# Performance work log

Measured on AMD Instinct MI355X. Metric: run time of the kernel, lower is better.

Reference implementation:

```python
import jax, jax.numpy as jnp
import numpy as np

B, C_IN, H, W = 2, 32, 512, 512
HIDDEN, SIZE = 768, 16
LATENT, NUM_CLASS = 128, 21
HP, WP = H // SIZE, W // SIZE
EPS = 1e-8
TEMP = 0.5


def setup_inputs() -> dict:
    key = jax.random.key(0)
    k1, k2, k3, k4, k5 = jax.random.split(key, 5)
    x = jax.random.normal(k1, (B, C_IN, H, W), dtype=jnp.float32)
    mask = jax.random.randint(k2, (B, NUM_CLASS, HP, WP), 0, 2).astype(jnp.int32)
    conv_w = jax.random.normal(k3, (HIDDEN, C_IN, SIZE, SIZE), dtype=jnp.float32) * 0.02
    conv_b = jax.random.normal(k4, (HIDDEN,), dtype=jnp.float32) * 0.02
    latent = jax.random.normal(k5, (1, LATENT * NUM_CLASS, HIDDEN), dtype=jnp.float32)
    return {"x": x, "mask": mask, "conv_w": conv_w, "conv_b": conv_b, "latent": latent}


def reference(x, mask, conv_w, conv_b, latent):
    # Patch embedding: Conv2d(kernel=stride=16) -> (B, HIDDEN, HP, WP)
    patch = jax.lax.conv_general_dilated(
        x, conv_w, window_strides=(SIZE, SIZE), padding='VALID',
        dimension_numbers=('NCHW', 'OIHW', 'NCHW'))
    patch = patch + conv_b[None, :, None, None]
    Bv = x.shape[0]
    N = HP * WP
    patch = patch.reshape(Bv, HIDDEN, N).transpose(0, 2, 1)  # (B, N, D)
    lat = jnp.broadcast_to(latent, (Bv, LATENT * NUM_CLASS, HIDDEN))  # (B, LC, D)

    # Cosine similarity as normalized batched matmul (same math as
    # torch CosineSimilarity over broadcast (B, LC, N, D))
    dots = jnp.einsum('bld,bnd->bln', lat, patch)  # (B, LC, N)
    lat_norm = jnp.linalg.norm(lat, axis=-1)       # (B, LC)
    pat_norm = jnp.linalg.norm(patch, axis=-1)     # (B, N)
    sim = dots / jnp.maximum(lat_norm[:, :, None] * pat_norm[:, None, :], EPS)

    sim = sim.reshape(Bv, LATENT, NUM_CLASS, HP, WP).mean(axis=1)  # (B, C, HP, WP)

    m = mask.astype(jnp.float32) >= 0.5
    s = jnp.sum(jnp.where(m, jnp.exp(sim / TEMP), 0.0))
    return -jnp.log(s)
```

## Files before the change

kernel.cpp:

```cpp
#include <hip/hip_runtime.h>
#include <math.h>

#define B_     2
#define CIN    32
#define HH     512
#define WW     512
#define HID    768
#define SZ     16
#define NPATCH 1024
#define KDIM   8192
#define NCLS   21
#define LAT    128
#define LC     2688
#define NP     (B_ * NPATCH)

#define NB_W4  1536
#define NB_XT  2048

typedef __attribute__((ext_vector_type(8))) short short8;
typedef __attribute__((ext_vector_type(4))) float f32x4;

__device__ __forceinline__ ushort f2bf(float f) {
    union { float f; unsigned u; } v; v.f = f;
    unsigned r = (v.u + 0x7fff + ((v.u >> 16) & 1)) >> 16;
    return (ushort)r;
}
__device__ __forceinline__ float bf2f(ushort u) {
    union { unsigned u; float f; } v; v.u = (unsigned)u << 16;
    return v.f;
}

__device__ __forceinline__ void gload16(const void* g, void* l) {
    __builtin_amdgcn_global_load_lds(
        (const __attribute__((address_space(1))) unsigned int*)g,
        (__attribute__((address_space(3))) unsigned int*)l, 16, 0, 0);
}

__global__ __launch_bounds__(256) void k_prep(const float* __restrict__ w,
                                              const float* __restrict__ x,
                                              const float* __restrict__ lat,
                                              ushort* __restrict__ wb,
                                              ushort* __restrict__ xb,
                                              float* __restrict__ classlat) {
    const int bid = blockIdx.x;
    const int t   = threadIdx.x;

    if (bid < NB_W4) {
#pragma unroll
        for (int k = 0; k < 4; ++k) {
            size_t i = ((size_t)bid * 1024 + k * 256 + t) * 4;
            float4 v = *(const float4*)(w + i);
            ushort4 o;
            o.x = f2bf(v.x); o.y = f2bf(v.y); o.z = f2bf(v.z); o.w = f2bf(v.w);
            *(ushort4*)(wb + i) = o;
        }
    } else if (bid < NB_W4 + NB_XT) {
        __shared__ ushort sh[32 * 264];
        const int cvb = bid - NB_W4;
        const int b  = cvb >> 10;
        const int c  = (cvb >> 5) & 31;
        const int ph = cvb & 31;
        const float* src = x + (((size_t)(b * CIN + c) * HH) + (size_t)ph * 16) * WW;

#pragma unroll
        for (int q = 0; q < 8; ++q) {
            int f  = q * 256 + t;
            int i  = f >> 7;
            int w4 = f & 127;
            float4 v = *(const float4*)(src + (size_t)i * WW + w4 * 4);
            int pw = w4 >> 2, j0 = (w4 & 3) * 4;
            ushort4 o;
            o.x = f2bf(v.x); o.y = f2bf(v.y); o.z = f2bf(v.z); o.w = f2bf(v.w);
            *(ushort4*)&sh[pw * 264 + i * 16 + j0] = o;
        }
        __syncthreads();

        ushort* dst = xb + ((size_t)(b * 1024 + ph * 32) << 13) + c * 256;
#pragma unroll
        for (int q = 0; q < 4; ++q) {
            int s  = q * 256 + t;
            int pw = s >> 5;
            int o8 = (s & 31) * 8;
            short8 v = *(const short8*)&sh[pw * 264 + o8];
            *(short8*)&dst[((size_t)pw << 13) + o8] = v;
        }
    } else {
        const int cls  = bid - (NB_W4 + NB_XT);
        const int lane = t & 63, wv = t >> 6;
        __shared__ float sc_sh[LAT];

        for (int q = 0; q < 32; q += 2) {
            int u0 = wv * 32 + q;
            const float* r0 = lat + (size_t)(u0 * NCLS + cls) * HID;
            const float* r1 = lat + (size_t)((u0 + 1) * NCLS + cls) * HID;
            float s0 = 0.f, s1 = 0.f;
#pragma unroll
            for (int e = 0; e < HID / 64; ++e) {
                float a = r0[lane + e * 64]; s0 += a * a;
                float b2 = r1[lane + e * 64]; s1 += b2 * b2;
            }
#pragma unroll
            for (int off = 32; off >= 1; off >>= 1) {
                s0 += __shfl_xor(s0, off, 64);
                s1 += __shfl_xor(s1, off, 64);
            }
            if (lane == 0) {
                sc_sh[u0]     = 1.0f / (128.0f * sqrtf(s0));
                sc_sh[u0 + 1] = 1.0f / (128.0f * sqrtf(s1));
            }
        }
        __syncthreads();

        float a0 = 0.f, a1 = 0.f, a2 = 0.f;
#pragma unroll 4
        for (int u = 0; u < LAT; ++u) {
            float sc = sc_sh[u];
            const float* row = lat + (size_t)(u * NCLS + cls) * HID;
            a0 += row[t] * sc;
            a1 += row[t + 256] * sc;
            a2 += row[t + 512] * sc;
        }
        classlat[cls * HID + t]       = a0;
        classlat[cls * HID + t + 256] = a1;
        classlat[cls * HID + t + 512] = a2;
    }
}

template <int SPLITK>
__global__ __launch_bounds__(256) void k_gemm(const ushort* __restrict__ xb,
                                              const ushort* __restrict__ wb,
                                              ushort* __restrict__ pbuf) {
    constexpr int KS = KDIM / SPLITK;
    __shared__ ushort Als[128 * 64];
    __shared__ ushort Bls[128 * 64];

    const int flat = blockIdx.x + 16 * (blockIdx.y + 6 * blockIdx.z);
    constexpr int nwg = 96 * SPLITK;
    const int wg = (flat & 7) * (nwg >> 3) + (flat >> 3);
    const int bz = wg / 96;
    const int rr = wg - bz * 96;
    const int by = rr % 6;
    const int bx = rr / 6;

    const int tid  = threadIdx.x;
    const int wv   = tid >> 6;
    const int lane = tid & 63;
    const int wm   = (wv >> 1) * 64;
    const int wn   = (wv & 1) * 64;

    const size_t abase = ((size_t)bx * 128) * KDIM + (size_t)bz * KS;
    const size_t bbase = ((size_t)by * 128) * KDIM + (size_t)bz * KS;

    const int srow  = wv * 8 + (lane >> 3);
    const int skoff = (((lane & 7) ^ (lane >> 3)) * 8);

    f32x4 acc[4][4];
#pragma unroll
    for (int m = 0; m < 4; ++m)
#pragma unroll
        for (int n = 0; n < 4; ++n) acc[m][n] = (f32x4)(0.f);

    const int fr = lane & 15, fq = lane >> 4;
    const int frx = (fr & 7) * 8;

    for (int kk = 0; kk < KS; kk += 64) {
#pragma unroll
        for (int q = 0; q < 4; ++q) {
            const int row = q * 32 + srow;
            gload16(&xb[abase + (size_t)row * KDIM + kk + skoff], &Als[q * 2048 + wv * 512]);
            gload16(&wb[bbase + (size_t)row * KDIM + kk + skoff], &Bls[q * 2048 + wv * 512]);
        }
        __syncthreads();

#pragma unroll
        for (int s = 0; s < 2; ++s) {
            short8 af[4], bf[4];
#pragma unroll
            for (int m = 0; m < 4; ++m)
                af[m] = *(const short8*)&Als[(wm + m * 16 + fr) * 64 + ((s * 32 + fq * 8) ^ frx)];
#pragma unroll
            for (int n = 0; n < 4; ++n)
                bf[n] = *(const short8*)&Bls[(wn + n * 16 + fr) * 64 + ((s * 32 + fq * 8) ^ frx)];
#pragma unroll
            for (int m = 0; m < 4; ++m)
#pragma unroll
                for (int n = 0; n < 4; ++n)
                    acc[m][n] = __builtin_amdgcn_mfma_f32_16x16x32_bf16(af[m], bf[n], acc[m][n], 0, 0, 0);
        }
        __syncthreads();
    }

#pragma unroll
    for (int m = 0; m < 4; ++m) {
#pragma unroll
        for (int n = 0; n < 4; ++n) {
            int col = by * 128 + wn + n * 16 + fr;
#pragma unroll
            for (int j = 0; j < 4; ++j) {
                int row = bx * 128 + wm + m * 16 + fq * 4 + j;
                pbuf[((size_t)row * SPLITK + bz) * HID + col] = f2bf(acc[m][n][j]);
            }
        }
    }
}

template <int SPLITK>
__global__ __launch_bounds__(256) void k_final(const ushort* __restrict__ pbuf,
                                               const float* __restrict__ conv_b,
                                               const float* __restrict__ classlat,
                                               const int* __restrict__ mask,
                                               float* __restrict__ partial) {
    const int p = blockIdx.x;
    const int b = p >> 10, n = p & 1023;
    const int t = threadIdx.x;
    const int lane = t & 63, wv = t >> 6;

    __shared__ ushort sh[SPLITK * HID];
    const ushort* pb = pbuf + (size_t)p * (SPLITK * HID);
    for (int i = t; i < SPLITK * HID / 8; i += 256)
        *(short8*)&sh[i * 8] = *(const short8*)&pb[(size_t)i * 8];
    __syncthreads();

    float f0 = conv_b[t], f1 = conv_b[t + 256], f2 = conv_b[t + 512];
#pragma unroll
    for (int z = 0; z < SPLITK; ++z) {
        f0 += bf2f(sh[z * HID + t]);
        f1 += bf2f(sh[z * HID + t + 256]);
        f2 += bf2f(sh[z * HID + t + 512]);
    }

    __shared__ float wsum[4];
    __shared__ float wdot[4][NCLS];
    __shared__ float cpart[NCLS];

    float ss = f0 * f0 + f1 * f1 + f2 * f2;
#pragma unroll
    for (int off = 32; off >= 1; off >>= 1) ss += __shfl_xor(ss, off, 64);
    if (lane == 0) wsum[wv] = ss;

    float dots[NCLS];
#pragma unroll
    for (int c = 0; c < NCLS; ++c) {
        const float* cl = classlat + c * HID;
        dots[c] = cl[t] * f0 + cl[t + 256] * f1 + cl[t + 512] * f2;
    }
#pragma unroll
    for (int c = 0; c < NCLS; ++c) {
        float v = dots[c];
#pragma unroll
        for (int off = 32; off >= 1; off >>= 1) v += __shfl_xor(v, off, 64);
        if (lane == 0) wdot[wv][c] = v;
    }
    __syncthreads();

    if (t < NCLS) {
        float tot  = wsum[0] + wsum[1] + wsum[2] + wsum[3];
        float invn = 1.0f / sqrtf(tot);
        float dot  = wdot[0][t] + wdot[1][t] + wdot[2][t] + wdot[3][t];
        float sim  = dot * invn;
        int   mv   = mask[(size_t)(b * NCLS + t) * NPATCH + n];
        cpart[t]   = (mv != 0) ? expf(sim * 2.0f) : 0.0f;
    }
    __syncthreads();
    if (t == 0) {
        float s = 0.f;
#pragma unroll
        for (int c = 0; c < NCLS; ++c) s += cpart[c];
        partial[p] = s;
    }
}

__global__ __launch_bounds__(256) void k_reduce(const float* __restrict__ partial,
                                                float* __restrict__ out) {
    int t = threadIdx.x;
    float s = 0.f;
    for (int i = t; i < NP; i += 256) s += partial[i];
#pragma unroll
    for (int off = 32; off >= 1; off >>= 1) s += __shfl_xor(s, off, 64);
    __shared__ float ws[4];
    if ((t & 63) == 0) ws[t >> 6] = s;
    __syncthreads();
    if (t == 0) out[0] = -logf(ws[0] + ws[1] + ws[2] + ws[3]);
}

extern "C" void kernel_launch(void* const* d_in, const int* in_sizes, int n_in,
                              void* d_out, int out_size, void* d_ws, size_t ws_size,
                              hipStream_t stream) {
    const float* x      = (const float*)d_in[0];
    const int*   mask   = (const int*)d_in[1];
    const float* conv_w = (const float*)d_in[2];
    const float* conv_b = (const float*)d_in[3];
    const float* latent = (const float*)d_in[4];
    float* out = (float*)d_out;

    const size_t xb_bytes   = (size_t)NP * KDIM * 2;
    const size_t wb_bytes   = (size_t)HID * KDIM * 2;
    const size_t pslice     = (size_t)NP * HID * 2;
    const size_t small_need = (size_t)NCLS * HID * 4 + NP * 4 + 256;

    char* base = (char*)d_ws;
    ushort* xb   = (ushort*)base;
    ushort* wb   = (ushort*)(base + xb_bytes);
    ushort* pbuf = (ushort*)(base + xb_bytes + wb_bytes);

    int splitk = 1;
    const size_t fixed = xb_bytes + wb_bytes + small_need;
    if (ws_size >= fixed + 8 * pslice)      splitk = 8;
    else if (ws_size >= fixed + 4 * pslice) splitk = 4;
    else if (ws_size >= fixed + 2 * pslice) splitk = 2;

    float* classlat = (float*)(base + xb_bytes + wb_bytes + (size_t)splitk * pslice);
    float* partial  = classlat + NCLS * HID;

    k_prep<<<NB_W4 + NB_XT + NCLS, 256, 0, stream>>>(conv_w, x, latent, wb, xb, classlat);

    dim3 g(NP / 128, HID / 128, splitk);
    switch (splitk) {
        case 8: k_gemm<8><<<g, 256, 0, stream>>>(xb, wb, pbuf); break;
        case 4: k_gemm<4><<<g, 256, 0, stream>>>(xb, wb, pbuf); break;
        case 2: k_gemm<2><<<g, 256, 0, stream>>>(xb, wb, pbuf); break;
        default: k_gemm<1><<<g, 256, 0, stream>>>(xb, wb, pbuf); break;
    }

    switch (splitk) {
        case 8: k_final<8><<<NP, 256, 0, stream>>>(pbuf, conv_b, classlat, mask, partial); break;
        case 4: k_final<4><<<NP, 256, 0, stream>>>(pbuf, conv_b, classlat, mask, partial); break;
        case 2: k_final<2><<<NP, 256, 0, stream>>>(pbuf, conv_b, classlat, mask, partial); break;
        default: k_final<1><<<NP, 256, 0, stream>>>(pbuf, conv_b, classlat, mask, partial); break;
    }
    k_reduce<<<1, 256, 0, stream>>>(partial, out);
}
```

Before: 95.84 us.

## Split latent norm into separate kernel and spread class reduction across more blocks

Moves the per-latent-row norm computation into a new k_scale kernel that handles 4 rows per block, so the class-latent reduction in k_prep no longer serially computes 128 norms per class. The class-latent averaging is split into 63 blocks (3 per class), scheduled first so the former tail blocks start early, and uses batched 8-wide loads. The weight and input conversion paths are reorganized to issue all global loads before converting, for more memory-level parallelism. The cost is one extra kernel launch and a small scale buffer in the workspace.

```diff
diff --git a/kernel.cpp b/kernel.cpp
--- a/kernel.cpp
+++ b/kernel.cpp
@@ -14,6 +14,7 @@
 #define LC     2688
 #define NP     (B_ * NPATCH)
 
+#define NB_CL  63
 #define NB_W4  1536
 #define NB_XT  2048
 
@@ -36,93 +37,108 @@
         (__attribute__((address_space(3))) unsigned int*)l, 16, 0, 0);
 }
 
+__global__ __launch_bounds__(256) void k_scale(const float* __restrict__ lat,
+                                               float* __restrict__ scale) {
+    int wid  = blockIdx.x * 4 + (threadIdx.x >> 6);
+    int lane = threadIdx.x & 63;
+    const float* row = lat + (size_t)wid * HID;
+    float s = 0.f;
+#pragma unroll
+    for (int q = 0; q < HID / 64; ++q) {
+        float v = row[lane + q * 64];
+        s += v * v;
+    }
+#pragma unroll
+    for (int off = 32; off >= 1; off >>= 1) s += __shfl_xor(s, off, 64);
+    if (lane == 0) scale[wid] = 1.0f / (128.0f * sqrtf(s));
+}
+
 __global__ __launch_bounds__(256) void k_prep(const float* __restrict__ w,
                                               const float* __restrict__ x,
                                               const float* __restrict__ lat,
+                                              const float* __restrict__ scale,
                                               ushort* __restrict__ wb,
                                               ushort* __restrict__ xb,
                                               float* __restrict__ classlat) {
     const int bid = blockIdx.x;
     const int t   = threadIdx.x;
 
-    if (bid < NB_W4) {
+    if (bid < NB_CL) {
+        const int cls  = bid / 3;
+        const int dseg = bid % 3;
+        __shared__ float sc_sh[LAT];
+        if (t < LAT) sc_sh[t] = scale[t * NCLS + cls];
+        __syncthreads();
+
+        const float* src = lat + (size_t)cls * HID + dseg * 256 + t;
+        float a = 0.f;
+        for (int u0 = 0; u0 < LAT; u0 += 8) {
+            float v[8];
+#pragma unroll
+            for (int q = 0; q < 8; ++q)
+                v[q] = src[(size_t)(u0 + q) * (NCLS * HID)];
+#pragma unroll
+            for (int q = 0; q < 8; ++q) a += v[q] * sc_sh[u0 + q];
+        }
+        classlat[cls * HID + dseg * 256 + t] = a;
+    } else if (bid < NB_CL + NB_W4) {
+        const int cb = bid - NB_CL;
+        float4 vv[4];
+#pragma unroll
+        for (int k = 0; k < 4; ++k)
+            vv[k] = *(const float4*)(w + ((size_t)cb * 1024 + k * 256 + t) * 4);
 #pragma unroll
         for (int k = 0; k < 4; ++k) {
-            size_t i = ((size_t)bid * 1024 + k * 256 + t) * 4;
-            float4 v = *(const float4*)(w + i);
             ushort4 o;
-            o.x = f2bf(v.x); o.y = f2bf(v.y); o.z = f2bf(v.z); o.w = f2bf(v.w);
-            *(ushort4*)(wb + i) = o;
-        }
-    } else if (bid < NB_W4 + NB_XT) {
+            o.x = f2bf(vv[k].x); o.y = f2bf(vv[k].y);
+            o.z = f2bf(vv[k].z); o.w = f2bf(vv[k].w);
+            *(ushort4*)(wb + ((size_t)cb * 1024 + k * 256 + t) * 4) = o;
+        }
+    } else {
         __shared__ ushort sh[32 * 264];
-        const int cvb = bid - NB_W4;
+        const int cvb = bid - (NB_CL + NB_W4);
         const int b  = cvb >> 10;
         const int c  = (cvb >> 5) & 31;
         const int ph = cvb & 31;
         const float* src = x + (((size_t)(b * CIN + c) * HH) + (size_t)ph * 16) * WW;
 
+        float4 vv[8];
 #pragma unroll
         for (int q = 0; q < 8; ++q) {
             int f  = q * 256 + t;
             int i  = f >> 7;
             int w4 = f & 127;
-            float4 v = *(const float4*)(src + (size_t)i * WW + w4 * 4);
+            vv[q] = *(const float4*)(src + (size_t)i * WW + w4 * 4);
+        }
+#pragma unroll
+        for (int q = 0; q < 8; ++q) {
+            int f  = q * 256 + t;
+            int i  = f >> 7;
+            int w4 = f & 127;
             int pw = w4 >> 2, j0 = (w4 & 3) * 4;
             ushort4 o;
-            o.x = f2bf(v.x); o.y = f2bf(v.y); o.z = f2bf(v.z); o.w = f2bf(v.w);
+            o.x = f2bf(vv[q].x); o.y = f2bf(vv[q].y);
+            o.z = f2bf(vv[q].z); o.w = f2bf(vv[q].w);
             *(ushort4*)&sh[pw * 264 + i * 16 + j0] = o;
         }
         __syncthreads();
 
         ushort* dst = xb + ((size_t)(b * 1024 + ph * 32) << 13) + c * 256;
+        short8 rv[4];
 #pragma unroll
         for (int q = 0; q < 4; ++q) {
             int s  = q * 256 + t;
             int pw = s >> 5;
             int o8 = (s & 31) * 8;
-            short8 v = *(const short8*)&sh[pw * 264 + o8];
-            *(short8*)&dst[((size_t)pw << 13) + o8] = v;
-        }
-    } else {
-        const int cls  = bid - (NB_W4 + NB_XT);
-        const int lane = t & 63, wv = t >> 6;
-        __shared__ float sc_sh[LAT];
-
-        for (int q = 0; q < 32; q += 2) {
-            int u0 = wv * 32 + q;
-            const float* r0 = lat + (size_t)(u0 * NCLS + cls) * HID;
-            const float* r1 = lat + (size_t)((u0 + 1) * NCLS + cls) * HID;
-            float s0 = 0.f, s1 = 0.f;
-#pragma unroll
-            for (int e = 0; e < HID / 64; ++e) {
-                float a = r0[lane + e * 64]; s0 += a * a;
-                float b2 = r1[lane + e * 64]; s1 += b2 * b2;
-            }
-#pragma unroll
-            for (int off = 32; off >= 1; off >>= 1) {
-                s0 += __shfl_xor(s0, off, 64);
-                s1 += __shfl_xor(s1, off, 64);
-            }
-            if (lane == 0) {
-                sc_sh[u0]     = 1.0f / (128.0f * sqrtf(s0));
-                sc_sh[u0 + 1] = 1.0f / (128.0f * sqrtf(s1));
-            }
-        }
-        __syncthreads();
-
-        float a0 = 0.f, a1 = 0.f, a2 = 0.f;
-#pragma unroll 4
-        for (int u = 0; u < LAT; ++u) {
-            float sc = sc_sh[u];
-            const float* row = lat + (size_t)(u * NCLS + cls) * HID;
-            a0 += row[t] * sc;
-            a1 += row[t + 256] * sc;
-            a2 += row[t + 512] * sc;
-        }
-        classlat[cls * HID + t]       = a0;
-        classlat[cls * HID + t + 256] = a1;
-        classlat[cls * HID + t + 512] = a2;
+            rv[q] = *(const short8*)&sh[pw * 264 + o8];
+        }
+#pragma unroll
+        for (int q = 0; q < 4; ++q) {
+            int s  = q * 256 + t;
+            int pw = s >> 5;
+            int o8 = (s & 31) * 8;
+            *(short8*)&dst[((size_t)pw << 13) + o8] = rv[q];
+        }
     }
 }
 
@@ -296,7 +312,7 @@
     const size_t xb_bytes   = (size_t)NP * KDIM * 2;
     const size_t wb_bytes   = (size_t)HID * KDIM * 2;
     const size_t pslice     = (size_t)NP * HID * 2;
-    const size_t small_need = (size_t)NCLS * HID * 4 + NP * 4 + 256;
+    const size_t small_need = (size_t)NCLS * HID * 4 + NP * 4 + LC * 4 + 256;
 
     char* base = (char*)d_ws;
     ushort* xb   = (ushort*)base;
@@ -311,8 +327,11 @@
 
     float* classlat = (float*)(base + xb_bytes + wb_bytes + (size_t)splitk * pslice);
     float* partial  = classlat + NCLS * HID;
-
-    k_prep<<<NB_W4 + NB_XT + NCLS, 256, 0, stream>>>(conv_w, x, latent, wb, xb, classlat);
+    float* scale    = partial + NP;
+
+    k_scale<<<LC / 4, 256, 0, stream>>>(latent, scale);
+    k_prep<<<NB_CL + NB_W4 + NB_XT, 256, 0, stream>>>(conv_w, x, latent, scale,
+                                                      wb, xb, classlat);
 
     dim3 g(NP / 128, HID / 128, splitk);
     switch (splitk) {
```

New measurement: 85.25 us. 1.12x faster.
